# Kernel optimization log

Measured on AMD Instinct MI355X. Metric: run time of the kernel, lower is better.

## Reference

```python
import jax, jax.numpy as jnp
import numpy as np

BIAS = 0.0001
TEMPERATURE = 1.0


def setup_inputs() -> dict:
    key = jax.random.key(0)
    k_h, k_w1, k_w2, k_u = jax.random.split(key, 4)
    N, H, Z = 8192, 64, 128
    h = jax.random.normal(k_h, (N, H), dtype=jnp.float32)
    W1 = jax.random.normal(k_w1, (H, H), dtype=jnp.float32) * (1.0 / np.sqrt(H))
    b1 = jnp.zeros((H,), dtype=jnp.float32)
    W2 = jax.random.normal(k_w2, (H, Z), dtype=jnp.float32) * (1.0 / np.sqrt(H))
    b2 = jnp.zeros((Z,), dtype=jnp.float32)
    noise_u = jax.random.uniform(k_u, (N, N), dtype=jnp.float32)
    return {"h": h, "W1": W1, "b1": b1, "W2": W2, "b2": b2, "noise_u": noise_u}


def reference(h, W1, b1, W2, b2, noise_u):
    # MLPA: Linear -> ReLU -> Linear, then outer-product adjacency logits
    Zmat = jnp.maximum(h @ W1 + b1, 0.0) @ W2 + b2          # [N, dim_z]
    adj_logits = Zmat @ Zmat.T                               # [N, N]
    # gumbel-sigmoid edge sampling (training path)
    eps = (2.0 * BIAS - 1.0) * noise_u + (1.0 - BIAS)        # uniform in [bias, 1-bias]
    gate = (jnp.log(eps) - jnp.log1p(-eps) + adj_logits) / TEMPERATURE
    adj = jax.nn.sigmoid(gate)
    # keep strict upper triangle, symmetrize
    adj = jnp.triu(adj, 1)
    adj = adj + adj.T
    # fill_diagonal_(1)
    N = adj.shape[0]
    idx = jnp.arange(N)
    adj = adj.at[idx, idx].set(1.0)
    # D^{-1/2} @ adj @ D^{-1/2} expressed as row/col rescale (same math)
    d = jnp.power(adj.sum(axis=1), -0.5)                     # [N]
    adj_norm = d[:, None] * adj * d[None, :]
    return adj_norm, adj_logits
```

## Files before the change

### kernel.cpp

```cpp
#include <hip/hip_runtime.h>
#include <hip/hip_bf16.h>
#include <math.h>

#define N 8192
#define ZD 128
#define NTILE 64
#define NUPPER 2080
#define AROW 136

typedef __attribute__((ext_vector_type(8))) _Float16 f16x8;
typedef __attribute__((ext_vector_type(4))) float f32x4;

__device__ __forceinline__ int tri_cum(int ti) {
    return (ti * (2 * NTILE + 1 - ti)) / 2;
}

__device__ __forceinline__ void tile_decode(int t, int& ti, int& tj) {
    int est = (int)((129.0f - sqrtf(16641.0f - 8.0f * (float)t)) * 0.5f);
    if (est < 0) est = 0;
    while (tri_cum(est) > t) --est;
    while (tri_cum(est + 1) <= t) ++est;
    ti = est;
    tj = est + (t - tri_cum(est));
}

__global__ __launch_bounds__(256) void k1_mlp(
    const float* __restrict__ h, const float* __restrict__ W1,
    const float* __restrict__ b1, const float* __restrict__ W2,
    const float* __restrict__ b2, _Float16* __restrict__ Zf)
{
    __shared__ float W1s[64][65];
    __shared__ float W2s[64][129];
    __shared__ float hs[32][68];
    __shared__ float Ts[32][68];
    __shared__ float b1s[64];
    __shared__ float b2s[128];
    const int tid = threadIdx.x;
    const int row0 = blockIdx.x * 32;

    for (int e = tid; e < 64 * 64; e += 256) W1s[e >> 6][e & 63] = W1[e];
    for (int e = tid; e < 64 * 128; e += 256) W2s[e >> 7][e & 127] = W2[e];
    for (int e = tid; e < 32 * 64; e += 256) hs[e >> 6][e & 63] = h[(size_t)row0 * 64 + e];
    if (tid < 64) b1s[tid] = b1[tid];
    if (tid < 128) b2s[tid] = b2[tid];
    __syncthreads();

    {
        const int c = tid & 63;
        const int r0 = (tid >> 6) * 8;
        float s[8];
        #pragma unroll
        for (int j = 0; j < 8; ++j) s[j] = b1s[c];
        #pragma unroll
        for (int k0 = 0; k0 < 64; k0 += 4) {
            const float w0 = W1s[k0 + 0][c], w1 = W1s[k0 + 1][c];
            const float w2 = W1s[k0 + 2][c], w3 = W1s[k0 + 3][c];
            #pragma unroll
            for (int j = 0; j < 8; ++j) {
                f32x4 hv = *(const f32x4*)&hs[r0 + j][k0];
                s[j] = fmaf(hv[0], w0, s[j]);
                s[j] = fmaf(hv[1], w1, s[j]);
                s[j] = fmaf(hv[2], w2, s[j]);
                s[j] = fmaf(hv[3], w3, s[j]);
            }
        }
        #pragma unroll
        for (int j = 0; j < 8; ++j) Ts[r0 + j][c] = fmaxf(s[j], 0.0f);
    }
    __syncthreads();
    {
        const int c = tid & 127;
        const int r0 = (tid >> 7) * 16;
        float s[16];
        #pragma unroll
        for (int j = 0; j < 16; ++j) s[j] = b2s[c];
        #pragma unroll
        for (int k0 = 0; k0 < 64; k0 += 4) {
            const float w0 = W2s[k0 + 0][c], w1 = W2s[k0 + 1][c];
            const float w2 = W2s[k0 + 2][c], w3 = W2s[k0 + 3][c];
            #pragma unroll
            for (int j = 0; j < 16; ++j) {
                f32x4 tv = *(const f32x4*)&Ts[r0 + j][k0];
                s[j] = fmaf(tv[0], w0, s[j]);
                s[j] = fmaf(tv[1], w1, s[j]);
                s[j] = fmaf(tv[2], w2, s[j]);
                s[j] = fmaf(tv[3], w3, s[j]);
            }
        }
        #pragma unroll
        for (int j = 0; j < 16; ++j)
            Zf[(size_t)(row0 + r0 + j) * ZD + c] = (_Float16)s[j];
    }
}

__global__ __launch_bounds__(256, 2) void k3_main(
    const _Float16* __restrict__ Zf, const float* __restrict__ noise,
    float* __restrict__ logits, unsigned char* __restrict__ vfull)
{
    int ti, tj;
    const int t = (blockIdx.x & 7) * (NUPPER / 8) + (blockIdx.x >> 3);
    tile_decode(t, ti, tj);
    const bool diag = (ti == tj);

    __shared__ _Float16 smem[2 * 128 * AROW];
    _Float16* As = smem;
    _Float16* Bs = smem + 128 * AROW;
    unsigned char* vTT = (unsigned char*)smem;
    unsigned char* vT  = (unsigned char*)(smem + 128 * AROW);

    const int tid = threadIdx.x;
    const int lane = tid & 63;
    const int w = tid >> 6;
    const int wr = w >> 1, wc = w & 1;
    const int fr = lane & 15;
    const int kg = lane >> 4;
    const int i0 = ti * 128, j0 = tj * 128;

    #pragma unroll
    for (int p = 0; p < 8; ++p) {
        const int c = tid + p * 256;
        const int row = c >> 4, cg = (c & 15) << 3;
        *(f16x8*)&As[row * AROW + cg] = *(const f16x8*)(Zf + (size_t)(i0 + row) * ZD + cg);
        *(f16x8*)&Bs[row * AROW + cg] = *(const f16x8*)(Zf + (size_t)(j0 + row) * ZD + cg);
    }
    __syncthreads();

    f32x4 acc[4][4];
    #pragma unroll
    for (int mf = 0; mf < 4; ++mf)
        #pragma unroll
        for (int nf = 0; nf < 4; ++nf)
            acc[mf][nf] = (f32x4)0.0f;

    #pragma unroll
    for (int kc = 0; kc < 4; ++kc) {
        const int ko = kc * 32 + kg * 8;
        f16x8 a[4], b[4];
        #pragma unroll
        for (int mf = 0; mf < 4; ++mf) {
            a[mf] = *(const f16x8*)&As[(wr * 64 + mf * 16 + fr) * AROW + ko];
            b[mf] = *(const f16x8*)&Bs[(wc * 64 + mf * 16 + fr) * AROW + ko];
        }
        #pragma unroll
        for (int mf = 0; mf < 4; ++mf)
            #pragma unroll
            for (int nf = 0; nf < 4; ++nf)
                acc[mf][nf] = __builtin_amdgcn_mfma_f32_16x16x32_f16(a[mf], b[nf], acc[mf][nf], 0, 0, 0);
    }
    __syncthreads();

    #pragma unroll
    for (int mf = 0; mf < 4; ++mf) {
        #pragma unroll
        for (int nf = 0; nf < 4; ++nf) {
            const int Rl = wr * 64 + mf * 16 + (lane >> 4) * 4;
            const int Cl = wc * 64 + nf * 16 + (lane & 15);
            const f32x4 Lv = acc[mf][nf];
            const size_t gi = (size_t)(i0 + Rl) * N + (j0 + Cl);
            #pragma unroll
            for (int k = 0; k < 4; ++k)
                __builtin_nontemporal_store(Lv[k], &logits[gi + (size_t)k * N]);
            __builtin_nontemporal_store(Lv, (f32x4*)&logits[(size_t)(j0 + Cl) * N + (i0 + Rl)]);
            unsigned q = 0;
            #pragma unroll
            for (int k = 0; k < 4; ++k) {
                float u = __builtin_nontemporal_load(&noise[gi + (size_t)k * N]);
                float eps = fmaf(-0.9998f, u, 0.9999f);
                float om  = fmaf( 0.9998f, u, 0.0001f);
                float gate = __logf(eps) - __logf(om) + Lv[k];
                float v = 1.0f / (1.0f + __expf(-gate));
                if (diag && (Rl + k) >= Cl) v = 0.0f;
                q |= ((unsigned)(int)rintf(v * 255.0f)) << (8 * k);
            }
            *(unsigned*)&vT[Cl * 132 + Rl] = q;
            #pragma unroll
            for (int k = 0; k < 4; ++k)
                vTT[(Rl + k) * 132 + Cl] = (unsigned char)((q >> (8 * k)) & 255);
        }
    }

    __syncthreads();

    if (!diag) {
        #pragma unroll
        for (int it = 0; it < 16; ++it) {
            const int idx = tid + it * 256;
            const int r = idx >> 5;
            const int c4 = (idx & 31) * 4;
            const unsigned q = *(const unsigned*)&vTT[r * 132 + c4];
            __builtin_nontemporal_store(q, (unsigned*)&vfull[(size_t)(i0 + r) * N + j0 + c4]);
        }
        #pragma unroll
        for (int it = 0; it < 16; ++it) {
            const int idx = tid + it * 256;
            const int c = idx >> 5;
            const int r4 = (idx & 31) * 4;
            const unsigned q = *(const unsigned*)&vT[c * 132 + r4];
            __builtin_nontemporal_store(q, (unsigned*)&vfull[(size_t)(j0 + c) * N + i0 + r4]);
        }
    } else {
        #pragma unroll
        for (int it = 0; it < 16; ++it) {
            const int idx = tid + it * 256;
            const int r = idx >> 5;
            const int c4 = (idx & 31) * 4;
            unsigned q = 0;
            #pragma unroll
            for (int e = 0; e < 4; ++e) {
                const int c = c4 + e;
                unsigned char b = (unsigned char)(vTT[r * 132 + c] | vTT[c * 132 + r]);
                q |= ((unsigned)b) << (8 * e);
            }
            __builtin_nontemporal_store(q, (unsigned*)&vfull[(size_t)(i0 + r) * N + j0 + c4]);
        }
    }
}

__global__ __launch_bounds__(256) void kE_sums(
    const unsigned char* __restrict__ vfull, float* __restrict__ dvec)
{
    const int row = blockIdx.x * 4 + (threadIdx.x >> 6);
    const int lane = threadIdx.x & 63;
    const unsigned* p = (const unsigned*)(vfull + (size_t)row * N);
    unsigned s = 0;
    #pragma unroll 8
    for (int k = 0; k < 32; ++k) {
        const unsigned q = __builtin_nontemporal_load(p + lane + k * 64);
        s += (q & 255) + ((q >> 8) & 255) + ((q >> 16) & 255) + (q >> 24);
    }
    #pragma unroll
    for (int off = 32; off >= 1; off >>= 1) s += __shfl_xor((int)s, off);
    if (lane == 0) dvec[row] = rsqrtf(1.0f + (float)s * (1.0f / 255.0f));
}

__global__ __launch_bounds__(256) void k5_norm(
    const unsigned char* __restrict__ vfull, float* __restrict__ adj,
    const float* __restrict__ dvec)
{
    const unsigned CHUNKS_PER_ROW = N / 4;
    const unsigned stride = gridDim.x * 256;
    const float inv255 = 1.0f / 255.0f;

    for (unsigned idx = blockIdx.x * 256 + threadIdx.x; idx < (unsigned)(N / 4) * N;
         idx += stride) {
        const unsigned row = idx / CHUNKS_PER_ROW;
        const unsigned col4 = (idx % CHUNKS_PER_ROW) * 4;
        const unsigned q = __builtin_nontemporal_load((const unsigned*)&vfull[(size_t)idx * 4]);
        const float sdi = dvec[row] * inv255;
        const f32x4 d4 = *(const f32x4*)&dvec[col4];
        f32x4 o;
        o[0] = (float)(q & 255)         * sdi * d4[0];
        o[1] = (float)((q >> 8) & 255)  * sdi * d4[1];
        o[2] = (float)((q >> 16) & 255) * sdi * d4[2];
        o[3] = (float)(q >> 24)         * sdi * d4[3];
        if (row - col4 < 4u) {
            const float di = dvec[row];
            o[row - col4] = di * di;
        }
        __builtin_nontemporal_store(o, (f32x4*)&adj[(size_t)idx * 4]);
    }
}

extern "C" void kernel_launch(void* const* d_in, const int* in_sizes, int n_in,
                              void* d_out, int out_size, void* d_ws, size_t ws_size,
                              hipStream_t stream)
{
    const float* h     = (const float*)d_in[0];
    const float* W1    = (const float*)d_in[1];
    const float* b1    = (const float*)d_in[2];
    const float* W2    = (const float*)d_in[3];
    const float* b2    = (const float*)d_in[4];
    const float* noise = (const float*)d_in[5];

    float* adj    = (float*)d_out;
    float* logits = adj + (size_t)N * N;

    _Float16* Zf         = (_Float16*)d_ws;
    unsigned char* vfull = (unsigned char*)(Zf + (size_t)N * ZD);
    float* dvec          = (float*)(vfull + (size_t)N * N);

    k1_mlp<<<256, 256, 0, stream>>>(h, W1, b1, W2, b2, Zf);
    k3_main<<<NUPPER, 256, 0, stream>>>(Zf, noise, logits, vfull);
    kE_sums<<<N / 4, 256, 0, stream>>>(vfull, dvec);
    k5_norm<<<4096, 256, 0, stream>>>(vfull, adj, dvec);
}
```

Before: 249.5 us.

## Launch full tile grid and read noise transposed instead of mirroring stores

The main kernel now launches all 64x64 tiles rather than only the upper triangle. Each tile writes its own logits and byte-adjacency block with coalesced stores, which removes the transposed mirror stores. Tiles below the diagonal stage the matching upper-triangle noise block through shared memory and read it transposed, so the sampled gate stays symmetric. In exchange the Z·Zᵀ MFMA work doubles and the upper-triangle noise is read twice, adding global read traffic.

Result: slower. 269.2 us (+7.9%).

```diff
diff --git a/kernel.cpp b/kernel.cpp
--- a/kernel.cpp
+++ b/kernel.cpp
@@ -5,24 +5,12 @@
 #define N 8192
 #define ZD 128
 #define NTILE 64
-#define NUPPER 2080
+#define NFULL 4096
 #define AROW 136
+#define NR 132
 
 typedef __attribute__((ext_vector_type(8))) _Float16 f16x8;
 typedef __attribute__((ext_vector_type(4))) float f32x4;
-
-__device__ __forceinline__ int tri_cum(int ti) {
-    return (ti * (2 * NTILE + 1 - ti)) / 2;
-}
-
-__device__ __forceinline__ void tile_decode(int t, int& ti, int& tj) {
-    int est = (int)((129.0f - sqrtf(16641.0f - 8.0f * (float)t)) * 0.5f);
-    if (est < 0) est = 0;
-    while (tri_cum(est) > t) --est;
-    while (tri_cum(est + 1) <= t) ++est;
-    ti = est;
-    tj = est + (t - tri_cum(est));
-}
 
 __global__ __launch_bounds__(256) void k1_mlp(
     const float* __restrict__ h, const float* __restrict__ W1,
@@ -97,16 +85,16 @@
     const _Float16* __restrict__ Zf, const float* __restrict__ noise,
     float* __restrict__ logits, unsigned char* __restrict__ vfull)
 {
-    int ti, tj;
-    const int t = (blockIdx.x & 7) * (NUPPER / 8) + (blockIdx.x >> 3);
-    tile_decode(t, ti, tj);
+    const int t = (blockIdx.x & 7) * (NFULL / 8) + (blockIdx.x >> 3);
+    const int ti = t >> 6, tj = t & 63;
     const bool diag = (ti == tj);
-
-    __shared__ _Float16 smem[2 * 128 * AROW];
-    _Float16* As = smem;
-    _Float16* Bs = smem + 128 * AROW;
-    unsigned char* vTT = (unsigned char*)smem;
-    unsigned char* vT  = (unsigned char*)(smem + 128 * AROW);
+    const bool lower = (ti > tj);
+
+    __shared__ char smem_raw[2 * 128 * AROW * 2];
+    _Float16* As = (_Float16*)smem_raw;
+    _Float16* Bs = As + 128 * AROW;
+    float* nz = (float*)smem_raw;
+    unsigned char* vTT = (unsigned char*)smem_raw;
 
     const int tid = threadIdx.x;
     const int lane = tid & 63;
@@ -149,6 +137,22 @@
     }
     __syncthreads();
 
+    {
+        const int rmin0 = lower ? j0 : i0;
+        const int cmax0 = lower ? i0 : j0;
+        #pragma unroll
+        for (int p = 0; p < 16; ++p) {
+            const int idx = tid + p * 256;
+            const int row = idx >> 5;
+            const int c4 = (idx & 31) * 4;
+            f32x4 u4 = __builtin_nontemporal_load(
+                (const f32x4*)&noise[(size_t)(rmin0 + row) * N + cmax0 + c4]);
+            *(f32x4*)&nz[row * NR + c4] = u4;
+        }
+    }
+    __syncthreads();
+
+    unsigned qv[4][4];
     #pragma unroll
     for (int mf = 0; mf < 4; ++mf) {
         #pragma unroll
@@ -160,11 +164,10 @@
             #pragma unroll
             for (int k = 0; k < 4; ++k)
                 __builtin_nontemporal_store(Lv[k], &logits[gi + (size_t)k * N]);
-            __builtin_nontemporal_store(Lv, (f32x4*)&logits[(size_t)(j0 + Cl) * N + (i0 + Rl)]);
             unsigned q = 0;
             #pragma unroll
             for (int k = 0; k < 4; ++k) {
-                float u = __builtin_nontemporal_load(&noise[gi + (size_t)k * N]);
+                const float u = lower ? nz[Cl * NR + (Rl + k)] : nz[(Rl + k) * NR + Cl];
                 float eps = fmaf(-0.9998f, u, 0.9999f);
                 float om  = fmaf( 0.9998f, u, 0.0001f);
                 float gate = __logf(eps) - __logf(om) + Lv[k];
@@ -172,47 +175,45 @@
                 if (diag && (Rl + k) >= Cl) v = 0.0f;
                 q |= ((unsigned)(int)rintf(v * 255.0f)) << (8 * k);
             }
-            *(unsigned*)&vT[Cl * 132 + Rl] = q;
-            #pragma unroll
-            for (int k = 0; k < 4; ++k)
-                vTT[(Rl + k) * 132 + Cl] = (unsigned char)((q >> (8 * k)) & 255);
-        }
-    }
-
-    __syncthreads();
-
-    if (!diag) {
-        #pragma unroll
-        for (int it = 0; it < 16; ++it) {
-            const int idx = tid + it * 256;
-            const int r = idx >> 5;
-            const int c4 = (idx & 31) * 4;
-            const unsigned q = *(const unsigned*)&vTT[r * 132 + c4];
-            __builtin_nontemporal_store(q, (unsigned*)&vfull[(size_t)(i0 + r) * N + j0 + c4]);
-        }
-        #pragma unroll
-        for (int it = 0; it < 16; ++it) {
-            const int idx = tid + it * 256;
-            const int c = idx >> 5;
-            const int r4 = (idx & 31) * 4;
-            const unsigned q = *(const unsigned*)&vT[c * 132 + r4];
-            __builtin_nontemporal_store(q, (unsigned*)&vfull[(size_t)(j0 + c) * N + i0 + r4]);
-        }
-    } else {
-        #pragma unroll
-        for (int it = 0; it < 16; ++it) {
-            const int idx = tid + it * 256;
-            const int r = idx >> 5;
-            const int c4 = (idx & 31) * 4;
-            unsigned q = 0;
-            #pragma unroll
-            for (int e = 0; e < 4; ++e) {
-                const int c = c4 + e;
-                unsigned char b = (unsigned char)(vTT[r * 132 + c] | vTT[c * 132 + r]);
-                q |= ((unsigned)b) << (8 * e);
-            }
-            __builtin_nontemporal_store(q, (unsigned*)&vfull[(size_t)(i0 + r) * N + j0 + c4]);
-        }
+            qv[mf][nf] = q;
+        }
+    }
+    __syncthreads();
+
+    #pragma unroll
+    for (int mf = 0; mf < 4; ++mf) {
+        #pragma unroll
+        for (int nf = 0; nf < 4; ++nf) {
+            const int Rl = wr * 64 + mf * 16 + (lane >> 4) * 4;
+            const int Cl = wc * 64 + nf * 16 + (lane & 15);
+            const unsigned q = qv[mf][nf];
+            if (!diag) {
+                #pragma unroll
+                for (int k = 0; k < 4; ++k)
+                    vTT[(Rl + k) * 132 + Cl] = (unsigned char)((q >> (8 * k)) & 255);
+            } else {
+                #pragma unroll
+                for (int k = 0; k < 4; ++k) {
+                    const int r = Rl + k;
+                    if (r < Cl) {
+                        const unsigned char b = (unsigned char)((q >> (8 * k)) & 255);
+                        vTT[r * 132 + Cl] = b;
+                        vTT[Cl * 132 + r] = b;
+                    }
+                }
+            }
+        }
+    }
+    if (diag && tid < 128) vTT[tid * 132 + tid] = 0;
+    __syncthreads();
+
+    #pragma unroll
+    for (int it = 0; it < 16; ++it) {
+        const int idx = tid + it * 256;
+        const int r = idx >> 5;
+        const int c4 = (idx & 31) * 4;
+        const unsigned q = *(const unsigned*)&vTT[r * 132 + c4];
+        __builtin_nontemporal_store(q, (unsigned*)&vfull[(size_t)(i0 + r) * N + j0 + c4]);
     }
 }
 
@@ -280,7 +281,7 @@
     float* dvec          = (float*)(vfull + (size_t)N * N);
 
     k1_mlp<<<256, 256, 0, stream>>>(h, W1, b1, W2, b2, Zf);
-    k3_main<<<NUPPER, 256, 0, stream>>>(Zf, noise, logits, vfull);
+    k3_main<<<NFULL, 256, 0, stream>>>(Zf, noise, logits, vfull);
     kE_sums<<<N / 4, 256, 0, stream>>>(vfull, dvec);
     k5_norm<<<4096, 256, 0, stream>>>(vfull, adj, dvec);
 }
```

## Fuse row-sum degree computation into main tile kernel via atomics

Applied to the files above, without the earlier changes.

Computes the adjacency row and column sums inside the main tile kernel using LDS atomics, then global atomics into a sums buffer that the MLP kernel initialises to 1. This removes the separate pass that re-read the full 64MB byte matrix to compute degrees. It also drops the LDS staging of the Z tiles in favour of direct global loads for the MFMA operands, which frees shared memory so occupancy can rise to 4 blocks per CU. The degree sums now use unquantised float values rather than the 8-bit quantised ones and float atomic ordering is nondeterministic, so results differ slightly.

Measured after the change: 320.6 us. 1.28x slower.

```diff
diff --git a/kernel.cpp b/kernel.cpp
--- a/kernel.cpp
+++ b/kernel.cpp
@@ -6,7 +6,6 @@
 #define ZD 128
 #define NTILE 64
 #define NUPPER 2080
-#define AROW 136
 
 typedef __attribute__((ext_vector_type(8))) _Float16 f16x8;
 typedef __attribute__((ext_vector_type(4))) float f32x4;
@@ -27,7 +26,8 @@
 __global__ __launch_bounds__(256) void k1_mlp(
     const float* __restrict__ h, const float* __restrict__ W1,
     const float* __restrict__ b1, const float* __restrict__ W2,
-    const float* __restrict__ b2, _Float16* __restrict__ Zf)
+    const float* __restrict__ b2, _Float16* __restrict__ Zf,
+    float* __restrict__ sums)
 {
     __shared__ float W1s[64][65];
     __shared__ float W2s[64][129];
@@ -38,6 +38,8 @@
     const int tid = threadIdx.x;
     const int row0 = blockIdx.x * 32;
 
+    if (tid < 32) sums[row0 + tid] = 1.0f;
+
     for (int e = tid; e < 64 * 64; e += 256) W1s[e >> 6][e & 63] = W1[e];
     for (int e = tid; e < 64 * 128; e += 256) W2s[e >> 7][e & 127] = W2[e];
     for (int e = tid; e < 32 * 64; e += 256) hs[e >> 6][e & 63] = h[(size_t)row0 * 64 + e];
@@ -93,20 +95,19 @@
     }
 }
 
-__global__ __launch_bounds__(256, 2) void k3_main(
+__global__ __launch_bounds__(256, 4) void k3_main(
     const _Float16* __restrict__ Zf, const float* __restrict__ noise,
-    float* __restrict__ logits, unsigned char* __restrict__ vfull)
+    float* __restrict__ logits, unsigned char* __restrict__ vfull,
+    float* __restrict__ sums)
 {
     int ti, tj;
     const int t = (blockIdx.x & 7) * (NUPPER / 8) + (blockIdx.x >> 3);
     tile_decode(t, ti, tj);
     const bool diag = (ti == tj);
 
-    __shared__ _Float16 smem[2 * 128 * AROW];
-    _Float16* As = smem;
-    _Float16* Bs = smem + 128 * AROW;
-    unsigned char* vTT = (unsigned char*)smem;
-    unsigned char* vT  = (unsigned char*)(smem + 128 * AROW);
+    __shared__ unsigned char vTT[128 * 132];
+    __shared__ unsigned char vT[128 * 132];
+    __shared__ float rs[128], cs[128];
 
     const int tid = threadIdx.x;
     const int lane = tid & 63;
@@ -116,14 +117,10 @@
     const int kg = lane >> 4;
     const int i0 = ti * 128, j0 = tj * 128;
 
-    #pragma unroll
-    for (int p = 0; p < 8; ++p) {
-        const int c = tid + p * 256;
-        const int row = c >> 4, cg = (c & 15) << 3;
-        *(f16x8*)&As[row * AROW + cg] = *(const f16x8*)(Zf + (size_t)(i0 + row) * ZD + cg);
-        *(f16x8*)&Bs[row * AROW + cg] = *(const f16x8*)(Zf + (size_t)(j0 + row) * ZD + cg);
-    }
-    __syncthreads();
+    if (tid < 128) { rs[tid] = 0.0f; cs[tid] = 0.0f; }
+
+    const _Float16* Ap = Zf + (size_t)(i0 + wr * 64) * ZD;
+    const _Float16* Bp = Zf + (size_t)(j0 + wc * 64) * ZD;
 
     f32x4 acc[4][4];
     #pragma unroll
@@ -138,8 +135,9 @@
         f16x8 a[4], b[4];
         #pragma unroll
         for (int mf = 0; mf < 4; ++mf) {
-            a[mf] = *(const f16x8*)&As[(wr * 64 + mf * 16 + fr) * AROW + ko];
-            b[mf] = *(const f16x8*)&Bs[(wc * 64 + mf * 16 + fr) * AROW + ko];
+            size_t off = (size_t)(mf * 16 + fr) * ZD + ko;
+            a[mf] = *(const f16x8*)(Ap + off);
+            b[mf] = *(const f16x8*)(Bp + off);
         }
         #pragma unroll
         for (int mf = 0; mf < 4; ++mf)
@@ -149,11 +147,13 @@
     }
     __syncthreads();
 
+    float cacc[4] = {0.f, 0.f, 0.f, 0.f};
     #pragma unroll
     for (int mf = 0; mf < 4; ++mf) {
+        const int Rl = wr * 64 + mf * 16 + (lane >> 4) * 4;
+        f32x4 rsum4 = (f32x4)0.0f;
         #pragma unroll
         for (int nf = 0; nf < 4; ++nf) {
-            const int Rl = wr * 64 + mf * 16 + (lane >> 4) * 4;
             const int Cl = wc * 64 + nf * 16 + (lane & 15);
             const f32x4 Lv = acc[mf][nf];
             const size_t gi = (size_t)(i0 + Rl) * N + (j0 + Cl);
@@ -171,13 +171,21 @@
                 float v = 1.0f / (1.0f + __expf(-gate));
                 if (diag && (Rl + k) >= Cl) v = 0.0f;
                 q |= ((unsigned)(int)rintf(v * 255.0f)) << (8 * k);
+                rsum4[k] += v;
+                cacc[nf] += v;
             }
             *(unsigned*)&vT[Cl * 132 + Rl] = q;
             #pragma unroll
             for (int k = 0; k < 4; ++k)
                 vTT[(Rl + k) * 132 + Cl] = (unsigned char)((q >> (8 * k)) & 255);
         }
-    }
+        #pragma unroll
+        for (int k = 0; k < 4; ++k)
+            atomicAdd(&rs[Rl + k], rsum4[k]);
+    }
+    #pragma unroll
+    for (int nf = 0; nf < 4; ++nf)
+        atomicAdd(&cs[wc * 64 + nf * 16 + (lane & 15)], cacc[nf]);
 
     __syncthreads();
 
@@ -198,6 +206,10 @@
             const unsigned q = *(const unsigned*)&vT[c * 132 + r4];
             __builtin_nontemporal_store(q, (unsigned*)&vfull[(size_t)(j0 + c) * N + i0 + r4]);
         }
+        if (tid < 128) {
+            atomicAdd(&sums[i0 + tid], rs[tid]);
+            atomicAdd(&sums[j0 + tid], cs[tid]);
+        }
     } else {
         #pragma unroll
         for (int it = 0; it < 16; ++it) {
@@ -213,24 +225,15 @@
             }
             __builtin_nontemporal_store(q, (unsigned*)&vfull[(size_t)(i0 + r) * N + j0 + c4]);
         }
-    }
-}
-
-__global__ __launch_bounds__(256) void kE_sums(
-    const unsigned char* __restrict__ vfull, float* __restrict__ dvec)
-{
-    const int row = blockIdx.x * 4 + (threadIdx.x >> 6);
-    const int lane = threadIdx.x & 63;
-    const unsigned* p = (const unsigned*)(vfull + (size_t)row * N);
-    unsigned s = 0;
-    #pragma unroll 8
-    for (int k = 0; k < 32; ++k) {
-        const unsigned q = __builtin_nontemporal_load(p + lane + k * 64);
-        s += (q & 255) + ((q >> 8) & 255) + ((q >> 16) & 255) + (q >> 24);
-    }
-    #pragma unroll
-    for (int off = 32; off >= 1; off >>= 1) s += __shfl_xor((int)s, off);
-    if (lane == 0) dvec[row] = rsqrtf(1.0f + (float)s * (1.0f / 255.0f));
+        if (tid < 128)
+            atomicAdd(&sums[i0 + tid], rs[tid] + cs[tid]);
+    }
+}
+
+__global__ void k4_dvec(const float* __restrict__ sums, float* __restrict__ dvec)
+{
+    int i = blockIdx.x * 256 + threadIdx.x;
+    if (i < N) dvec[i] = rsqrtf(sums[i]);
 }
 
 __global__ __launch_bounds__(256) void k5_norm(
@@ -277,10 +280,11 @@
 
     _Float16* Zf         = (_Float16*)d_ws;
     unsigned char* vfull = (unsigned char*)(Zf + (size_t)N * ZD);
-    float* dvec          = (float*)(vfull + (size_t)N * N);
-
-    k1_mlp<<<256, 256, 0, stream>>>(h, W1, b1, W2, b2, Zf);
-    k3_main<<<NUPPER, 256, 0, stream>>>(Zf, noise, logits, vfull);
-    kE_sums<<<N / 4, 256, 0, stream>>>(vfull, dvec);
+    float* sums          = (float*)(vfull + (size_t)N * N);
+    float* dvec          = sums + N;
+
+    k1_mlp<<<256, 256, 0, stream>>>(h, W1, b1, W2, b2, Zf, sums);
+    k3_main<<<NUPPER, 256, 0, stream>>>(Zf, noise, logits, vfull, sums);
+    k4_dvec<<<32, 256, 0, stream>>>(sums, dvec);
     k5_norm<<<4096, 256, 0, stream>>>(vfull, adj, dvec);
 }
```
